# Kernel tuning notes

Measured on AMD Instinct MI355X. Metric: run time of the kernel, lower is better.

## Reference

```python
import jax, jax.numpy as jnp
import numpy as np


def setup_inputs() -> dict:
    key = jax.random.key(0)
    ks = jax.random.split(key, 5)
    B, S, C, H = 32, 512, 320, 512
    scale = 1.0 / np.sqrt(H)
    return {
        "x": jax.random.normal(ks[0], (B, S, C), dtype=jnp.float32),
        "w_ih": jax.random.normal(ks[1], (4 * H, S), dtype=jnp.float32) * scale,
        "w_hh": jax.random.normal(ks[2], (4 * H, H), dtype=jnp.float32) * scale,
        "b_ih": jax.random.normal(ks[3], (4 * H,), dtype=jnp.float32) * scale,
        "b_hh": jax.random.normal(ks[4], (4 * H,), dtype=jnp.float32) * scale,
    }


def reference(x, w_ih, w_hh, b_ih, b_hh):
    # x: (B, S, C). Original permutes to (B, C, S) and runs a length-1 LSTM per
    # channel with zero initial state -> single LSTM cell step:
    #   gates = x_c @ W_ih^T + b_ih + b_hh   (W_hh @ h0 == 0)
    # PyTorch gate order: i, f, g, o.
    B, S, C = x.shape
    H = w_hh.shape[1]
    gates = jnp.einsum("bsc,gs->bcg", x, w_ih) + b_ih + b_hh  # (B, C, 4H)
    i_g, f_g, g_g, o_g = jnp.split(gates, 4, axis=-1)
    c = jax.nn.sigmoid(i_g) * jnp.tanh(g_g)           # c0 = 0
    h = jax.nn.sigmoid(o_g) * jnp.tanh(c)             # (B, C, H)
    # Faithful to torch: cat over channels along batch dim -> (C*B, H),
    # then reshape to (B, C, H) (scrambles batch/channel order).
    h = jnp.transpose(h, (1, 0, 2)).reshape(B, C, H)
    # dropout is identity in eval mode
    return jnp.transpose(h, (0, 2, 1))                # (B, H, C)
```

## Files before the change

### kernel.cpp

```cpp
#include <hip/hip_runtime.h>
#include <stdint.h>

#define B_  32
#define S_  512
#define C_  320
#define H_  512

typedef __attribute__((ext_vector_type(8))) short short8;
typedef __attribute__((ext_vector_type(4))) float f32x4;

__device__ __forceinline__ unsigned short f2bf(float x){
  unsigned u = __builtin_bit_cast(unsigned, x);
  u = u + 0x7FFFu + ((u >> 16) & 1u);
  return (unsigned short)(u >> 16);
}
__device__ __forceinline__ float sigf(float x){ return 1.0f/(1.0f + __expf(-x)); }
__device__ __forceinline__ float tanh_fast(float x){ return 2.0f/(1.0f + __expf(-2.0f*x)) - 1.0f; }

__device__ __forceinline__ void gload16(const void* g, void* l){
  __builtin_amdgcn_global_load_lds((const __attribute__((address_space(1))) void*)g,
                                   (__attribute__((address_space(3))) void*)l, 16, 0, 0);
}

__global__ __launch_bounds__(256) void k_prep(const float* __restrict__ w,
                                              const float* __restrict__ x,
                                              unsigned short* __restrict__ aws,
                                              unsigned short* __restrict__ xws){
  const int bidg = blockIdx.x;
  const int tid = threadIdx.x;
  if (bidg < 768){
    int flat = bidg*256 + tid;
    int plane = flat >> 16;
    int rem   = flat & 65535;
    int srow  = (plane == 0 ? 0 : (plane == 1 ? 1024 : 1536));
    float4 v = ((const float4*)w)[srow*128 + rem];
    uint2 p;
    p.x = (unsigned)f2bf(v.x) | ((unsigned)f2bf(v.y) << 16);
    p.y = (unsigned)f2bf(v.z) | ((unsigned)f2bf(v.w) << 16);
    ((uint2*)aws)[flat] = p;
    return;
  }
  __shared__ float lds[64][65];
  const int idx = bidg - 768;
  const int st = idx & 7;
  const int r5 = idx >> 3;
  const int ctt = r5 % 5, b = r5 / 5;
  const int s0 = st*64, c0 = ctt*64;
  const int row = tid >> 2, q = tid & 3;

  const float* src = x + ((size_t)(b*S_ + s0 + row))*C_ + c0 + q*16;
  #pragma unroll
  for (int j = 0; j < 4; j++){
    float4 v = ((const float4*)src)[j];
    lds[row][q*16 + j*4 + 0] = v.x;
    lds[row][q*16 + j*4 + 1] = v.y;
    lds[row][q*16 + j*4 + 2] = v.z;
    lds[row][q*16 + j*4 + 3] = v.w;
  }
  __syncthreads();
  const int wr2 = tid >> 3;
  const int l8  = tid & 7;
  #pragma unroll
  for (int half = 0; half < 2; half++){
    const int crow = half*32 + wr2;
    const size_t nprime = (size_t)(c0 + crow)*32 + (size_t)b;
    short8 o;
    #pragma unroll
    for (int e = 0; e < 8; e++)
      o[e] = (short)f2bf(lds[l8*8 + e][crow]);
    *(short8*)(xws + nprime*S_ + s0 + l8*8) = o;
  }
}

__global__ __launch_bounds__(256) void k_gemm(const unsigned short* __restrict__ aws,
                                              const unsigned short* __restrict__ xws,
                                              const float* __restrict__ b_ih,
                                              const float* __restrict__ b_hh,
                                              float* __restrict__ out){
  __shared__ alignas(16) char lds[163840];

  const int tid  = threadIdx.x;
  const int w    = tid >> 6;
  const int lane = tid & 63;
  const int wm = w >> 1, wn = w & 1;

  const int bid = blockIdx.x;
  const int x8 = bid & 7, y = bid >> 3;
  const int mt = y & 15, g = y >> 4;
  const int nt = g*8 + x8;
  const int k0 = mt*32;
  const int nbase = nt*64;

  f32x4 acc[3][2];
  #pragma unroll
  for (int gi = 0; gi < 3; gi++)
    #pragma unroll
    for (int nf = 0; nf < 2; nf++)
      acc[gi][nf] = (f32x4){0.f, 0.f, 0.f, 0.f};

  const char* wsb = (const char*)aws;
  {
    #pragma unroll
    for (int i = 0; i < 24; i++){
      const int q = i*4 + w;
      const int gi = q >> 5, row = q & 31;
      const int slot = (lane << 4) ^ ((row & 7) << 4);
      const unsigned src = (unsigned)((gi*512 + k0 + row)*1024) + (unsigned)slot;
      gload16(wsb + (size_t)src, &lds[0] + gi*32768 + row*1024);
    }
    #pragma unroll
    for (int i = 0; i < 16; i++){
      const int row = i*4 + w;
      const int slot = (lane << 4) ^ ((row & 7) << 4);
      const unsigned src = 2097152u + (unsigned)((nbase + row)*1024) + (unsigned)slot;
      gload16(wsb + (size_t)src, &lds[0] + 98304 + row*1024);
    }
  }
  __syncthreads();

  const int l15  = lane & 15;
  const int hi16 = (lane >> 4) << 4;
  const int xkey = (l15 & 7) << 4;
  const int arow = wm*16 + l15;
  const int brow0 = wn*32 + l15;

  #pragma unroll
  for (int ks = 0; ks < 16; ks++){
    const int colb = (ks*64 + hi16) ^ xkey;
    short8 aF[3], bF[2];
    #pragma unroll
    for (int gi = 0; gi < 3; gi++)
      aF[gi] = *(const short8*)(&lds[0] + gi*32768 + arow*1024 + colb);
    #pragma unroll
    for (int nf = 0; nf < 2; nf++)
      bF[nf] = *(const short8*)(&lds[0] + 98304 + (brow0 + nf*16)*1024 + colb);
    #pragma unroll
    for (int gi = 0; gi < 3; gi++)
      #pragma unroll
      for (int nf = 0; nf < 2; nf++)
        acc[gi][nf] = __builtin_amdgcn_mfma_f32_16x16x32_bf16(aF[gi], bF[nf], acc[gi][nf], 0, 0, 0);
  }
  __syncthreads();

  float* tr = (float*)&lds[0];
  {
    const int kbl = wm*16 + ((lane >> 4) << 2);
    const int kg  = k0 + kbl;
    float bi[4], bg[4], bo[4];
    #pragma unroll
    for (int r = 0; r < 4; r++){
      bi[r] = b_ih[kg + r]        + b_hh[kg + r];
      bg[r] = b_ih[1024 + kg + r] + b_hh[1024 + kg + r];
      bo[r] = b_ih[1536 + kg + r] + b_hh[1536 + kg + r];
    }
    #pragma unroll
    for (int nf = 0; nf < 2; nf++){
      const int nl = wn*32 + nf*16 + l15;
      #pragma unroll
      for (int r = 0; r < 4; r++){
        float iv = acc[0][nf][r] + bi[r];
        float gv = acc[1][nf][r] + bg[r];
        float ov = acc[2][nf][r] + bo[r];
        float ce = sigf(iv) * tanh_fast(gv);
        tr[(kbl + r)*68 + nl] = sigf(ov) * tanh_fast(ce);
      }
    }
  }
  __syncthreads();

  const int klo   = tid >> 3;
  const int lane8 = tid & 7;
  const size_t rowoff = (size_t)(k0 + klo)*C_;
  #pragma unroll
  for (int j = 0; j < 2; j++){
    const int nl0 = j*32 + lane8*4;
    const int ng  = nbase + nl0;
    const int b2  = ng / 320;
    const int c2  = ng - b2*320;
    float4 v;
    v.x = tr[klo*68 + nl0 + 0];
    v.y = tr[klo*68 + nl0 + 1];
    v.z = tr[klo*68 + nl0 + 2];
    v.w = tr[klo*68 + nl0 + 3];
    *(float4*)(out + (size_t)b2*(H_*C_) + rowoff + c2) = v;
  }
}

extern "C" void kernel_launch(void* const* d_in, const int* in_sizes, int n_in,
                              void* d_out, int out_size, void* d_ws, size_t ws_size,
                              hipStream_t stream){
  const float* x    = (const float*)d_in[0];
  const float* w_ih = (const float*)d_in[1];
  const float* b_ih = (const float*)d_in[3];
  const float* b_hh = (const float*)d_in[4];
  float* out = (float*)d_out;

  char* ws = (char*)d_ws;
  unsigned short* aws = (unsigned short*)(ws);
  unsigned short* xws = (unsigned short*)(ws + 2097152);

  k_prep <<<2048, 256, 0, stream>>>(w_ih, x, aws, xws);
  k_gemm <<<2560, 256, 0, stream>>>(aws, xws, b_ih, b_hh, out);
}
```

Before: 58.82 us.

## Fuse prep and GEMM into one persistent kernel with a grid barrier

Merges the weight/input bf16 conversion kernel and the GEMM kernel into a single persistent launch of 256 blocks. A global atomic barrier separates the two phases. Each block keeps its weight tile resident in LDS and loops over 10 N-tiles, so the A tile is loaded once instead of being reloaded per tile. This removes a kernel launch and repeated A loads, but adds a memset, a spin barrier, and serialised per-tile load/compute with no overlap. It also cuts the grid to 256 blocks at occupancy 1.

```diff
diff --git a/kernel.cpp b/kernel.cpp
--- a/kernel.cpp
+++ b/kernel.cpp
@@ -9,10 +9,10 @@
 typedef __attribute__((ext_vector_type(8))) short short8;
 typedef __attribute__((ext_vector_type(4))) float f32x4;
 
-__device__ __forceinline__ unsigned short f2bf(float x){
+__device__ __forceinline__ unsigned f2bf(float x){
   unsigned u = __builtin_bit_cast(unsigned, x);
   u = u + 0x7FFFu + ((u >> 16) & 1u);
-  return (unsigned short)(u >> 16);
+  return u >> 16;
 }
 __device__ __forceinline__ float sigf(float x){ return 1.0f/(1.0f + __expf(-x)); }
 __device__ __forceinline__ float tanh_fast(float x){ return 2.0f/(1.0f + __expf(-2.0f*x)) - 1.0f; }
@@ -22,137 +22,153 @@
                                    (__attribute__((address_space(3))) void*)l, 16, 0, 0);
 }
 
-__global__ __launch_bounds__(256) void k_prep(const float* __restrict__ w,
-                                              const float* __restrict__ x,
-                                              unsigned short* __restrict__ aws,
-                                              unsigned short* __restrict__ xws){
-  const int bidg = blockIdx.x;
+__global__ __launch_bounds__(256, 1) void k_fused(const float* __restrict__ w,
+                                                  const float* __restrict__ x,
+                                                  const float* __restrict__ b_ih,
+                                                  const float* __restrict__ b_hh,
+                                                  unsigned short* __restrict__ aws,
+                                                  unsigned short* __restrict__ xws,
+                                                  unsigned* __restrict__ bar,
+                                                  float* __restrict__ out){
+  __shared__ union {
+    float t[64][65];
+    char  raw[163840];
+  } sm;
+
+  const int bid = blockIdx.x;
   const int tid = threadIdx.x;
-  if (bidg < 768){
-    int flat = bidg*256 + tid;
+
+  #pragma unroll
+  for (int i = 0; i < 3; i++){
+    int flat  = (bid*3 + i)*256 + tid;
     int plane = flat >> 16;
     int rem   = flat & 65535;
     int srow  = (plane == 0 ? 0 : (plane == 1 ? 1024 : 1536));
     float4 v = ((const float4*)w)[srow*128 + rem];
     uint2 p;
-    p.x = (unsigned)f2bf(v.x) | ((unsigned)f2bf(v.y) << 16);
-    p.y = (unsigned)f2bf(v.z) | ((unsigned)f2bf(v.w) << 16);
+    p.x = f2bf(v.x) | (f2bf(v.y) << 16);
+    p.y = f2bf(v.z) | (f2bf(v.w) << 16);
     ((uint2*)aws)[flat] = p;
-    return;
-  }
-  __shared__ float lds[64][65];
-  const int idx = bidg - 768;
-  const int st = idx & 7;
-  const int r5 = idx >> 3;
-  const int ctt = r5 % 5, b = r5 / 5;
-  const int s0 = st*64, c0 = ctt*64;
-  const int row = tid >> 2, q = tid & 3;
-
-  const float* src = x + ((size_t)(b*S_ + s0 + row))*C_ + c0 + q*16;
+  }
+
+  for (int jj = 0; jj < 5; jj++){
+    const int idx = bid*5 + jj;
+    const int st = idx & 7;
+    const int r5 = idx >> 3;
+    const int ctt = r5 % 5, b = r5 / 5;
+    const int s0 = st*64, c0 = ctt*64;
+    const int row = tid >> 2, q = tid & 3;
+
+    const float* src = x + ((size_t)(b*S_ + s0 + row))*C_ + c0 + q*16;
+    #pragma unroll
+    for (int j = 0; j < 4; j++){
+      float4 v = ((const float4*)src)[j];
+      sm.t[row][q*16 + j*4 + 0] = v.x;
+      sm.t[row][q*16 + j*4 + 1] = v.y;
+      sm.t[row][q*16 + j*4 + 2] = v.z;
+      sm.t[row][q*16 + j*4 + 3] = v.w;
+    }
+    __syncthreads();
+    const int wr2 = tid >> 3;
+    const int l8  = tid & 7;
+    #pragma unroll
+    for (int half = 0; half < 2; half++){
+      const int crow = half*32 + wr2;
+      const size_t nprime = (size_t)(c0 + crow)*32 + (size_t)b;
+      short8 o;
+      #pragma unroll
+      for (int e = 0; e < 8; e++)
+        o[e] = (short)f2bf(sm.t[l8*8 + e][crow]);
+      *(short8*)(xws + nprime*S_ + s0 + l8*8) = o;
+    }
+    __syncthreads();
+  }
+
+  __threadfence();
+  __syncthreads();
+  if (tid == 0){
+    __hip_atomic_fetch_add(bar, 1u, __ATOMIC_ACQ_REL, __HIP_MEMORY_SCOPE_AGENT);
+    while (__hip_atomic_load(bar, __ATOMIC_ACQUIRE, __HIP_MEMORY_SCOPE_AGENT) < 256u)
+      __builtin_amdgcn_s_sleep(32);
+  }
+  __syncthreads();
+
+  const int w_   = tid >> 6;
+  const int lane = tid & 63;
+  const int wm = w_ >> 1, wn = w_ & 1;
+  const int mt = bid >> 4;
+  const int ng = bid & 15;
+  const int k0 = mt*32;
+
+  const char* wsb = (const char*)aws;
+
   #pragma unroll
-  for (int j = 0; j < 4; j++){
-    float4 v = ((const float4*)src)[j];
-    lds[row][q*16 + j*4 + 0] = v.x;
-    lds[row][q*16 + j*4 + 1] = v.y;
-    lds[row][q*16 + j*4 + 2] = v.z;
-    lds[row][q*16 + j*4 + 3] = v.w;
-  }
-  __syncthreads();
-  const int wr2 = tid >> 3;
-  const int l8  = tid & 7;
+  for (int i = 0; i < 24; i++){
+    const int q  = i*4 + w_;
+    const int gi = q >> 5, row = q & 31;
+    const int slot = (lane << 4) ^ ((row & 7) << 4);
+    const unsigned src = (unsigned)((gi*512 + k0 + row)*1024 + slot);
+    gload16(wsb + (size_t)src, sm.raw + gi*32768 + row*1024);
+  }
+
+  const int kbl = wm*16 + ((lane >> 4) << 2);
+  const int kg  = k0 + kbl;
+  float bi[4], bg[4], bo[4];
   #pragma unroll
-  for (int half = 0; half < 2; half++){
-    const int crow = half*32 + wr2;
-    const size_t nprime = (size_t)(c0 + crow)*32 + (size_t)b;
-    short8 o;
-    #pragma unroll
-    for (int e = 0; e < 8; e++)
-      o[e] = (short)f2bf(lds[l8*8 + e][crow]);
-    *(short8*)(xws + nprime*S_ + s0 + l8*8) = o;
-  }
-}
-
-__global__ __launch_bounds__(256) void k_gemm(const unsigned short* __restrict__ aws,
-                                              const unsigned short* __restrict__ xws,
-                                              const float* __restrict__ b_ih,
-                                              const float* __restrict__ b_hh,
-                                              float* __restrict__ out){
-  __shared__ alignas(16) char lds[163840];
-
-  const int tid  = threadIdx.x;
-  const int w    = tid >> 6;
-  const int lane = tid & 63;
-  const int wm = w >> 1, wn = w & 1;
-
-  const int bid = blockIdx.x;
-  const int x8 = bid & 7, y = bid >> 3;
-  const int mt = y & 15, g = y >> 4;
-  const int nt = g*8 + x8;
-  const int k0 = mt*32;
-  const int nbase = nt*64;
-
-  f32x4 acc[3][2];
-  #pragma unroll
-  for (int gi = 0; gi < 3; gi++)
-    #pragma unroll
-    for (int nf = 0; nf < 2; nf++)
-      acc[gi][nf] = (f32x4){0.f, 0.f, 0.f, 0.f};
-
-  const char* wsb = (const char*)aws;
-  {
-    #pragma unroll
-    for (int i = 0; i < 24; i++){
-      const int q = i*4 + w;
-      const int gi = q >> 5, row = q & 31;
+  for (int r = 0; r < 4; r++){
+    bi[r] = b_ih[kg + r]        + b_hh[kg + r];
+    bg[r] = b_ih[1024 + kg + r] + b_hh[1024 + kg + r];
+    bo[r] = b_ih[1536 + kg + r] + b_hh[1536 + kg + r];
+  }
+
+  const int l15   = lane & 15;
+  const int hi16  = (lane >> 4) << 4;
+  const int xkey  = (l15 & 7) << 4;
+  const int arow  = wm*16 + l15;
+  const int brow0 = wn*32 + l15;
+  const int klo   = tid >> 3;
+  const int lane8 = tid & 7;
+  const size_t rowoff = (size_t)(k0 + klo)*C_;
+
+  for (int it = 0; it < 10; it++){
+    const int nt = ng*10 + it;
+    const int nbase = nt*64;
+
+    #pragma unroll
+    for (int i = 0; i < 16; i++){
+      const int row = i*4 + w_;
       const int slot = (lane << 4) ^ ((row & 7) << 4);
-      const unsigned src = (unsigned)((gi*512 + k0 + row)*1024) + (unsigned)slot;
-      gload16(wsb + (size_t)src, &lds[0] + gi*32768 + row*1024);
-    }
-    #pragma unroll
-    for (int i = 0; i < 16; i++){
-      const int row = i*4 + w;
-      const int slot = (lane << 4) ^ ((row & 7) << 4);
-      const unsigned src = 2097152u + (unsigned)((nbase + row)*1024) + (unsigned)slot;
-      gload16(wsb + (size_t)src, &lds[0] + 98304 + row*1024);
-    }
-  }
-  __syncthreads();
-
-  const int l15  = lane & 15;
-  const int hi16 = (lane >> 4) << 4;
-  const int xkey = (l15 & 7) << 4;
-  const int arow = wm*16 + l15;
-  const int brow0 = wn*32 + l15;
-
-  #pragma unroll
-  for (int ks = 0; ks < 16; ks++){
-    const int colb = (ks*64 + hi16) ^ xkey;
-    short8 aF[3], bF[2];
+      const unsigned src = 2097152u + (unsigned)((nbase + row)*1024 + slot);
+      gload16(wsb + (size_t)src, sm.raw + 98304 + row*1024);
+    }
+    __syncthreads();
+
+    f32x4 acc[3][2];
     #pragma unroll
     for (int gi = 0; gi < 3; gi++)
-      aF[gi] = *(const short8*)(&lds[0] + gi*32768 + arow*1024 + colb);
-    #pragma unroll
-    for (int nf = 0; nf < 2; nf++)
-      bF[nf] = *(const short8*)(&lds[0] + 98304 + (brow0 + nf*16)*1024 + colb);
-    #pragma unroll
-    for (int gi = 0; gi < 3; gi++)
       #pragma unroll
       for (int nf = 0; nf < 2; nf++)
-        acc[gi][nf] = __builtin_amdgcn_mfma_f32_16x16x32_bf16(aF[gi], bF[nf], acc[gi][nf], 0, 0, 0);
-  }
-  __syncthreads();
-
-  float* tr = (float*)&lds[0];
-  {
-    const int kbl = wm*16 + ((lane >> 4) << 2);
-    const int kg  = k0 + kbl;
-    float bi[4], bg[4], bo[4];
-    #pragma unroll
-    for (int r = 0; r < 4; r++){
-      bi[r] = b_ih[kg + r]        + b_hh[kg + r];
-      bg[r] = b_ih[1024 + kg + r] + b_hh[1024 + kg + r];
-      bo[r] = b_ih[1536 + kg + r] + b_hh[1536 + kg + r];
-    }
+        acc[gi][nf] = (f32x4){0.f, 0.f, 0.f, 0.f};
+
+    #pragma unroll
+    for (int ks = 0; ks < 16; ks++){
+      const int colb = (ks*64 + hi16) ^ xkey;
+      short8 aF[3], bF[2];
+      #pragma unroll
+      for (int gi = 0; gi < 3; gi++)
+        aF[gi] = *(const short8*)(sm.raw + gi*32768 + arow*1024 + colb);
+      #pragma unroll
+      for (int nf = 0; nf < 2; nf++)
+        bF[nf] = *(const short8*)(sm.raw + 98304 + (brow0 + nf*16)*1024 + colb);
+      #pragma unroll
+      for (int gi = 0; gi < 3; gi++)
+        #pragma unroll
+        for (int nf = 0; nf < 2; nf++)
+          acc[gi][nf] = __builtin_amdgcn_mfma_f32_16x16x32_bf16(aF[gi], bF[nf], acc[gi][nf], 0, 0, 0);
+    }
+    __syncthreads();
+
+    float* tr = (float*)(sm.raw + 98304);
     #pragma unroll
     for (int nf = 0; nf < 2; nf++){
       const int nl = wn*32 + nf*16 + l15;
@@ -165,24 +181,22 @@
         tr[(kbl + r)*68 + nl] = sigf(ov) * tanh_fast(ce);
       }
     }
-  }
-  __syncthreads();
-
-  const int klo   = tid >> 3;
-  const int lane8 = tid & 7;
-  const size_t rowoff = (size_t)(k0 + klo)*C_;
-  #pragma unroll
-  for (int j = 0; j < 2; j++){
-    const int nl0 = j*32 + lane8*4;
-    const int ng  = nbase + nl0;
-    const int b2  = ng / 320;
-    const int c2  = ng - b2*320;
-    float4 v;
-    v.x = tr[klo*68 + nl0 + 0];
-    v.y = tr[klo*68 + nl0 + 1];
-    v.z = tr[klo*68 + nl0 + 2];
-    v.w = tr[klo*68 + nl0 + 3];
-    *(float4*)(out + (size_t)b2*(H_*C_) + rowoff + c2) = v;
+    __syncthreads();
+
+    #pragma unroll
+    for (int j = 0; j < 2; j++){
+      const int nl0 = j*32 + lane8*4;
+      const int ngl = nbase + nl0;
+      const int b2  = ngl / 320;
+      const int c2  = ngl - b2*320;
+      float4 v;
+      v.x = tr[klo*68 + nl0 + 0];
+      v.y = tr[klo*68 + nl0 + 1];
+      v.z = tr[klo*68 + nl0 + 2];
+      v.w = tr[klo*68 + nl0 + 3];
+      *(float4*)(out + (size_t)b2*(H_*C_) + rowoff + c2) = v;
+    }
+    __syncthreads();
   }
 }
 
@@ -198,7 +212,8 @@
   char* ws = (char*)d_ws;
   unsigned short* aws = (unsigned short*)(ws);
   unsigned short* xws = (unsigned short*)(ws + 2097152);
-
-  k_prep <<<2048, 256, 0, stream>>>(w_ih, x, aws, xws);
-  k_gemm <<<2560, 256, 0, stream>>>(aws, xws, b_ih, b_hh, out);
-}
+  unsigned* bar = (unsigned*)(ws + 12582912);
+
+  hipMemsetAsync(bar, 0, 4, stream);
+  k_fused<<<256, 256, 0, stream>>>(w_ih, x, b_ih, b_hh, aws, xws, bar, out);
+}
```

After: 123.0 us. 2.09x slower.
